# Kernel tuning notes

Hardware: AMD Instinct MI355X
Metric: run time of the kernel (lower is better)

## Reference

```python
import jax, jax.numpy as jnp
import numpy as np

N_NODES = 100000
N_EDGES = 3200000
IN_DIM = 128


def setup_inputs() -> dict:
    key = jax.random.key(0)
    ks = jax.random.split(key, 6)
    x = jax.random.normal(ks[0], (N_NODES, IN_DIM), dtype=jnp.float32)
    edge_index = jax.random.randint(ks[1], (2, N_EDGES), 0, N_NODES, dtype=jnp.int64)
    # Glorot-ish init for weights, zero bias (PyG GCNConv default has bias)
    W1 = jax.random.normal(ks[2], (IN_DIM, 32), dtype=jnp.float32) / np.sqrt(IN_DIM)
    b1 = jnp.zeros((32,), dtype=jnp.float32)
    W2 = jax.random.normal(ks[3], (32, 16), dtype=jnp.float32) / np.sqrt(32.0)
    b2 = jnp.zeros((16,), dtype=jnp.float32)
    Wf = jax.random.normal(ks[4], (16, 1), dtype=jnp.float32) / np.sqrt(16.0)
    bf = jnp.zeros((1,), dtype=jnp.float32)
    return {"x": x, "edge_index": edge_index, "W1": W1, "b1": b1,
            "W2": W2, "b2": b2, "Wf": Wf, "bf": bf}


def reference(x, edge_index, W1, b1, W2, b2, Wf, bf):
    N = x.shape[0]
    # PyG GCNConv: add self-loops, symmetric normalization D^-1/2 (A+I) D^-1/2
    loop = jnp.arange(N, dtype=edge_index.dtype)
    src = jnp.concatenate([edge_index[0], loop])  # message sources (x_j)
    dst = jnp.concatenate([edge_index[1], loop])  # aggregation targets
    deg = jax.ops.segment_sum(jnp.ones_like(dst, dtype=x.dtype), dst, num_segments=N)
    dinv = jax.lax.rsqrt(jnp.maximum(deg, 1.0))  # deg >= 1 due to self-loops
    norm = dinv[src] * dinv[dst]                  # per-edge coefficient

    def gcn_conv(h, W, b):
        h = h @ W                                 # linear transform first (small dim)
        msg = h[src] * norm[:, None]              # gather + scale
        return jax.ops.segment_sum(msg, dst, num_segments=N) + b  # scatter-add

    h = jax.nn.relu(gcn_conv(x, W1, b1))
    h = jax.nn.relu(gcn_conv(h, W2, b2))
    return (h @ Wf + bf).squeeze(-1)              # [N]
```

## Files before the change

### kernel.cpp

```cpp
#include <hip/hip_runtime.h>


#define TPB 256
#define NBUCK 256
#define BCAP 16384
#define CHUNK 8192

__device__ __forceinline__ unsigned f2bf(float f) {
    unsigned u = __float_as_uint(f);
    return (u + 0x7FFFu + ((u >> 16) & 1u)) >> 16;
}
__device__ __forceinline__ float bflo(unsigned u) { return __uint_as_float(u << 16); }
__device__ __forceinline__ float bfhi(unsigned u) { return __uint_as_float(u & 0xFFFF0000u); }

__global__ void zero_bcursor_kernel(int* __restrict__ bcur) {
    bcur[threadIdx.x] = 0;
}

__global__ __launch_bounds__(256) void binA2_kernel(
        const int* __restrict__ src, const int* __restrict__ dst,
        int* __restrict__ bcur, unsigned* __restrict__ staging, int E, int NPB) {
    __shared__ unsigned packed[CHUNK];
    __shared__ unsigned char buckb[CHUNK];
    __shared__ int hist[NBUCK];
    __shared__ int scan_[NBUCK];
    __shared__ int lstart[NBUCK];
    __shared__ int lcur[NBUCK];
    __shared__ int gbase[NBUCK];
    int tid = threadIdx.x;
    int start = blockIdx.x * CHUNK;
    int sz = min(CHUNK, E - start);

    hist[tid] = 0;
    __syncthreads();
    for (int i = tid; i < sz; i += 256) {
        unsigned d = (unsigned)dst[start + i];
        atomicAdd(&hist[d / (unsigned)NPB], 1);
    }
    __syncthreads();
    int v = hist[tid];
    scan_[tid] = v;
    __syncthreads();
    for (int dd = 1; dd < NBUCK; dd <<= 1) {
        int t = 0;
        if (tid >= dd) t = scan_[tid - dd];
        __syncthreads();
        scan_[tid] += t;
        __syncthreads();
    }
    lstart[tid] = scan_[tid] - v;
    lcur[tid] = 0;
    gbase[tid] = atomicAdd(&bcur[tid], v);
    __syncthreads();
    for (int i = tid; i < sz; i += 256) {
        unsigned d = (unsigned)dst[start + i];
        unsigned s = (unsigned)src[start + i];
        unsigned b = d / (unsigned)NPB;
        unsigned loc = d - b * (unsigned)NPB;
        int pos = atomicAdd(&lcur[b], 1);
        int si = lstart[b] + pos;
        packed[si] = (loc << 20) | s;
        buckb[si] = (unsigned char)b;
    }
    __syncthreads();
    for (int i = tid; i < sz; i += 256) {
        unsigned b = buckb[i];
        int dsti = gbase[b] + (i - lstart[b]);
        if (dsti < BCAP)
            staging[(size_t)b * BCAP + dsti] = packed[i];
    }
}

__global__ void bucket_scan_kernel(const int* __restrict__ bcur, int* __restrict__ bbase) {
    __shared__ int s[NBUCK];
    int tid = threadIdx.x;
    int v = min(bcur[tid], BCAP);
    s[tid] = v;
    __syncthreads();
    for (int d = 1; d < NBUCK; d <<= 1) {
        int t = 0;
        if (tid >= d) t = s[tid - d];
        __syncthreads();
        s[tid] += t;
        __syncthreads();
    }
    bbase[tid] = s[tid] - v;
}

__global__ void buildB_kernel(const int* __restrict__ bcur, const int* __restrict__ bbase,
                              const unsigned* __restrict__ staging,
                              int* __restrict__ offs, int* __restrict__ counts,
                              float* __restrict__ dinv, int* __restrict__ csr_src,
                              int N, int NPB) {
    __shared__ int hist[512];
    __shared__ int scan_[512];
    __shared__ int cur[512];
    int b = blockIdx.x;
    int tid = threadIdx.x;
    int sz = min(bcur[b], BCAP);
    int base = bbase[b];
    int n0 = b * NPB;
    int nn = min(NPB, N - n0);
    const unsigned* se = staging + (size_t)b * BCAP;

    hist[tid] = 0;
    __syncthreads();
    for (int i = tid; i < sz; i += 512)
        atomicAdd(&hist[se[i] >> 20], 1);
    __syncthreads();
    int h = hist[tid];
    scan_[tid] = h;
    __syncthreads();
    for (int d = 1; d < 512; d <<= 1) {
        int t = 0;
        if (tid >= d) t = scan_[tid - d];
        __syncthreads();
        scan_[tid] += t;
        __syncthreads();
    }
    int excl = scan_[tid] - h;
    cur[tid] = excl;
    if (tid < nn) {
        int node = n0 + tid;
        offs[node] = base + excl;
        counts[node] = h;
        dinv[node] = rsqrtf((float)(h + 1));
    }
    __syncthreads();
    for (int i = tid; i < sz; i += 512) {
        unsigned p = se[i];
        int pos = atomicAdd(&cur[p >> 20], 1);
        csr_src[base + pos] = (int)(p & 0xFFFFFu);
    }
}

__global__ __launch_bounds__(256) void gemm1_kernel(
        const float* __restrict__ x, const float* __restrict__ W1,
        const float* __restrict__ dinv, unsigned* __restrict__ xwd, int N) {
    __shared__ float ws_[128 * 32];
    for (int i = threadIdx.x; i < 128 * 32; i += blockDim.x) ws_[i] = W1[i];
    __syncthreads();
    int t = threadIdx.x;
    int node = blockIdx.x * 64 + (t >> 2);
    if (node >= N) return;
    int jq = (t & 3) * 8;
    float acc[8];
#pragma unroll
    for (int j = 0; j < 8; ++j) acc[j] = 0.0f;
    const float4* xr = (const float4*)(x + (size_t)node * 128);
#pragma unroll 4
    for (int k4 = 0; k4 < 32; ++k4) {
        float4 xv = xr[k4];
        const float* wb = ws_ + (k4 * 4) * 32 + jq;
        float4 a0 = *(const float4*)(wb);
        float4 a1 = *(const float4*)(wb + 4);
        float4 b0 = *(const float4*)(wb + 32);
        float4 b1v = *(const float4*)(wb + 36);
        float4 c0 = *(const float4*)(wb + 64);
        float4 c1 = *(const float4*)(wb + 68);
        float4 d0 = *(const float4*)(wb + 96);
        float4 d1 = *(const float4*)(wb + 100);
        acc[0] += xv.x * a0.x + xv.y * b0.x + xv.z * c0.x + xv.w * d0.x;
        acc[1] += xv.x * a0.y + xv.y * b0.y + xv.z * c0.y + xv.w * d0.y;
        acc[2] += xv.x * a0.z + xv.y * b0.z + xv.z * c0.z + xv.w * d0.z;
        acc[3] += xv.x * a0.w + xv.y * b0.w + xv.z * c0.w + xv.w * d0.w;
        acc[4] += xv.x * a1.x + xv.y * b1v.x + xv.z * c1.x + xv.w * d1.x;
        acc[5] += xv.x * a1.y + xv.y * b1v.y + xv.z * c1.y + xv.w * d1.y;
        acc[6] += xv.x * a1.z + xv.y * b1v.z + xv.z * c1.z + xv.w * d1.z;
        acc[7] += xv.x * a1.w + xv.y * b1v.w + xv.z * c1.w + xv.w * d1.w;
    }
    float d = dinv[node];
    unsigned pk0 = f2bf(acc[0] * d) | (f2bf(acc[1] * d) << 16);
    unsigned pk1 = f2bf(acc[2] * d) | (f2bf(acc[3] * d) << 16);
    unsigned pk2 = f2bf(acc[4] * d) | (f2bf(acc[5] * d) << 16);
    unsigned pk3 = f2bf(acc[6] * d) | (f2bf(acc[7] * d) << 16);
    ((uint4*)(xwd + (size_t)node * 16))[t & 3] = make_uint4(pk0, pk1, pk2, pk3);
}

__global__ __launch_bounds__(256) void aggS32_kernel(
        const int* __restrict__ offs, const int* __restrict__ counts,
        const int* __restrict__ csr_src, const float* __restrict__ dinv,
        const unsigned* __restrict__ xwd, float* __restrict__ agg, int N) {
    int t = threadIdx.x;
    int q = t & 3;
    int node = blockIdx.x * 64 + (t >> 2);
    if (node >= N) return;
    int off = offs[node];
    int deg = counts[node];
    float acc[8];
    {
        uint4 v = ((const uint4*)(xwd + (size_t)node * 16))[q];
        acc[0] = bflo(v.x); acc[1] = bfhi(v.x);
        acc[2] = bflo(v.y); acc[3] = bfhi(v.y);
        acc[4] = bflo(v.z); acc[5] = bfhi(v.z);
        acc[6] = bflo(v.w); acc[7] = bfhi(v.w);
    }
    int i = 0;
    for (; i + 1 < deg; i += 2) {
        int s0 = csr_src[off + i];
        int s1 = csr_src[off + i + 1];
        uint4 v0 = ((const uint4*)(xwd + (size_t)s0 * 16))[q];
        uint4 v1 = ((const uint4*)(xwd + (size_t)s1 * 16))[q];
        acc[0] += bflo(v0.x) + bflo(v1.x); acc[1] += bfhi(v0.x) + bfhi(v1.x);
        acc[2] += bflo(v0.y) + bflo(v1.y); acc[3] += bfhi(v0.y) + bfhi(v1.y);
        acc[4] += bflo(v0.z) + bflo(v1.z); acc[5] += bfhi(v0.z) + bfhi(v1.z);
        acc[6] += bflo(v0.w) + bflo(v1.w); acc[7] += bfhi(v0.w) + bfhi(v1.w);
    }
    if (i < deg) {
        int s = csr_src[off + i];
        uint4 v = ((const uint4*)(xwd + (size_t)s * 16))[q];
        acc[0] += bflo(v.x); acc[1] += bfhi(v.x);
        acc[2] += bflo(v.y); acc[3] += bfhi(v.y);
        acc[4] += bflo(v.z); acc[5] += bfhi(v.z);
        acc[6] += bflo(v.w); acc[7] += bfhi(v.w);
    }
    float dv = dinv[node];
    float* op = agg + (size_t)node * 32 + q * 8;
    ((float4*)op)[0] = make_float4(acc[0] * dv, acc[1] * dv, acc[2] * dv, acc[3] * dv);
    ((float4*)op)[1] = make_float4(acc[4] * dv, acc[5] * dv, acc[6] * dv, acc[7] * dv);
}

__global__ void gemm2_kernel(const float* __restrict__ agg1, const float* __restrict__ W2,
                             const float* __restrict__ b1, const float* __restrict__ dinv,
                             unsigned* __restrict__ h2wd, int N) {
    __shared__ float ws_[32 * 16];
    __shared__ float bs_[32];
    for (int i = threadIdx.x; i < 32 * 16; i += blockDim.x) ws_[i] = W2[i];
    if (threadIdx.x < 32) bs_[threadIdx.x] = b1[threadIdx.x];
    __syncthreads();
    int node = blockIdx.x * blockDim.x + threadIdx.x;
    if (node >= N) return;
    float h[32];
    const float4* ar = (const float4*)(agg1 + (size_t)node * 32);
#pragma unroll
    for (int k4 = 0; k4 < 8; ++k4) {
        float4 v = ar[k4];
        h[k4 * 4 + 0] = fmaxf(v.x + bs_[k4 * 4 + 0], 0.0f);
        h[k4 * 4 + 1] = fmaxf(v.y + bs_[k4 * 4 + 1], 0.0f);
        h[k4 * 4 + 2] = fmaxf(v.z + bs_[k4 * 4 + 2], 0.0f);
        h[k4 * 4 + 3] = fmaxf(v.w + bs_[k4 * 4 + 3], 0.0f);
    }
    float acc[16];
#pragma unroll
    for (int j = 0; j < 16; ++j) acc[j] = 0.0f;
#pragma unroll
    for (int k = 0; k < 32; ++k) {
        float hv = h[k];
#pragma unroll
        for (int j4 = 0; j4 < 4; ++j4) {
            float4 w = *(const float4*)(ws_ + k * 16 + j4 * 4);
            acc[j4 * 4 + 0] += hv * w.x;
            acc[j4 * 4 + 1] += hv * w.y;
            acc[j4 * 4 + 2] += hv * w.z;
            acc[j4 * 4 + 3] += hv * w.w;
        }
    }
    float d = dinv[node];
    unsigned pk[8];
#pragma unroll
    for (int j = 0; j < 8; ++j)
        pk[j] = f2bf(acc[2 * j] * d) | (f2bf(acc[2 * j + 1] * d) << 16);
    uint4* hp = (uint4*)(h2wd + (size_t)node * 8);
    hp[0] = make_uint4(pk[0], pk[1], pk[2], pk[3]);
    hp[1] = make_uint4(pk[4], pk[5], pk[6], pk[7]);
}

__global__ __launch_bounds__(256) void aggS16f_kernel(
        const int* __restrict__ offs, const int* __restrict__ counts,
        const int* __restrict__ csr_src, const float* __restrict__ dinv,
        const unsigned* __restrict__ h2wd,
        const float* __restrict__ b2, const float* __restrict__ Wf,
        const float* __restrict__ bf, float* __restrict__ out, int N) {
    __shared__ float bs_[16];
    __shared__ float wf_[16];
    __shared__ float bfv;
    int t = threadIdx.x;
    if (t < 16) { bs_[t] = b2[t]; wf_[t] = Wf[t]; }
    if (t == 0) bfv = bf[0];
    __syncthreads();
    int q = t & 1;
    int node = blockIdx.x * 128 + (t >> 1);
    if (node >= N) return;
    int off = offs[node];
    int deg = counts[node];
    float acc[8];
    {
        uint4 v = ((const uint4*)(h2wd + (size_t)node * 8))[q];
        acc[0] = bflo(v.x); acc[1] = bfhi(v.x);
        acc[2] = bflo(v.y); acc[3] = bfhi(v.y);
        acc[4] = bflo(v.z); acc[5] = bfhi(v.z);
        acc[6] = bflo(v.w); acc[7] = bfhi(v.w);
    }
    int i = 0;
    for (; i + 1 < deg; i += 2) {
        int s0 = csr_src[off + i];
        int s1 = csr_src[off + i + 1];
        uint4 v0 = ((const uint4*)(h2wd + (size_t)s0 * 8))[q];
        uint4 v1 = ((const uint4*)(h2wd + (size_t)s1 * 8))[q];
        acc[0] += bflo(v0.x) + bflo(v1.x); acc[1] += bfhi(v0.x) + bfhi(v1.x);
        acc[2] += bflo(v0.y) + bflo(v1.y); acc[3] += bfhi(v0.y) + bfhi(v1.y);
        acc[4] += bflo(v0.z) + bflo(v1.z); acc[5] += bfhi(v0.z) + bfhi(v1.z);
        acc[6] += bflo(v0.w) + bflo(v1.w); acc[7] += bfhi(v0.w) + bfhi(v1.w);
    }
    if (i < deg) {
        int s = csr_src[off + i];
        uint4 v = ((const uint4*)(h2wd + (size_t)s * 8))[q];
        acc[0] += bflo(v.x); acc[1] += bfhi(v.x);
        acc[2] += bflo(v.y); acc[3] += bfhi(v.y);
        acc[4] += bflo(v.z); acc[5] += bfhi(v.z);
        acc[6] += bflo(v.w); acc[7] += bfhi(v.w);
    }
    float dv = dinv[node];
    const float* bq = bs_ + q * 8;
    const float* wq = wf_ + q * 8;
    float part = 0.f;
#pragma unroll
    for (int k = 0; k < 8; ++k)
        part += fmaxf(acc[k] * dv + bq[k], 0.f) * wq[k];
    part += __shfl_xor(part, 1, 64);
    if (q == 0) out[node] = part + bfv;
}

extern "C" void kernel_launch(void* const* d_in, const int* in_sizes, int n_in,
                              void* d_out, int out_size, void* d_ws, size_t ws_size,
                              hipStream_t stream) {
    const float* x  = (const float*)d_in[0];
    const int*   ei = (const int*)d_in[1];
    const float* W1 = (const float*)d_in[2];
    const float* b1 = (const float*)d_in[3];
    const float* W2 = (const float*)d_in[4];
    const float* b2 = (const float*)d_in[5];
    const float* Wf = (const float*)d_in[6];
    const float* bf = (const float*)d_in[7];

    int N = in_sizes[0] / 128;
    int E = in_sizes[1] / 2;
    const int* src = ei;
    const int* dst = ei + E;
    int NPB = (N + NBUCK - 1) / NBUCK;

    size_t Np = ((size_t)N + 3) & ~(size_t)3;
    size_t Ep = ((size_t)E + 3) & ~(size_t)3;
    int* wsI      = (int*)d_ws;
    int* counts   = wsI;
    int* offs     = counts + Np;
    int* bcur     = offs + Np;
    int* bbase    = bcur + NBUCK;
    int* csr_src  = bbase + NBUCK;
    float* dinv   = (float*)(csr_src + Ep);
    unsigned* xwd = (unsigned*)(dinv + Np);
    float* agg1   = (float*)(xwd + 16 * Np);
    unsigned* h2wd= (unsigned*)(agg1 + 32 * Np);
    float* out    = (float*)d_out;
    unsigned* staging = (unsigned*)agg1;

    int nbG1 = (N + 63) / 64;
    int nbC  = (E + CHUNK - 1) / CHUNK;
    int nbN  = (N + TPB - 1) / TPB;
    int nbA32 = (N + 63) / 64;
    int nbA16 = (N + 127) / 128;

    zero_bcursor_kernel<<<1, NBUCK, 0, stream>>>(bcur);
    binA2_kernel<<<nbC, 256, 0, stream>>>(src, dst, bcur, staging, E, NPB);
    bucket_scan_kernel<<<1, NBUCK, 0, stream>>>(bcur, bbase);
    buildB_kernel<<<NBUCK, 512, 0, stream>>>(bcur, bbase, staging, offs, counts,
                                             dinv, csr_src, N, NPB);
    gemm1_kernel<<<nbG1, 256, 0, stream>>>(x, W1, dinv, xwd, N);
    aggS32_kernel<<<nbA32, 256, 0, stream>>>(offs, counts, csr_src, dinv, xwd, agg1, N);
    gemm2_kernel<<<nbN, TPB, 0, stream>>>(agg1, W2, b1, dinv, h2wd, N);
    aggS16f_kernel<<<nbA16, 256, 0, stream>>>(offs, counts, csr_src, dinv, h2wd,
                                              b2, Wf, bf, out, N);
}
```

Before: 284.9 us.

## Split layer-1 features into two half arrays and aggregate each in a separate pass

Gemm1 now writes the 32-wide bf16 projected features as two 16-wide arrays, and layer-1 aggregation runs twice, once per half, with 2 threads per node. Each half array is 3.2 MB rather than 6.4 MB, so the random gathers should hit L2 more often, at the cost of reading the CSR index lists twice. The bucket prefix scan is folded into each buildB block, and the zeroing kernel is replaced by a memset, removing two small launches.

```diff
diff --git a/kernel.cpp b/kernel.cpp
--- a/kernel.cpp
+++ b/kernel.cpp
@@ -12,10 +12,6 @@
 }
 __device__ __forceinline__ float bflo(unsigned u) { return __uint_as_float(u << 16); }
 __device__ __forceinline__ float bfhi(unsigned u) { return __uint_as_float(u & 0xFFFF0000u); }
-
-__global__ void zero_bcursor_kernel(int* __restrict__ bcur) {
-    bcur[threadIdx.x] = 0;
-}
 
 __global__ __launch_bounds__(256) void binA2_kernel(
         const int* __restrict__ src, const int* __restrict__ dst,
@@ -71,34 +67,28 @@
     }
 }
 
-__global__ void bucket_scan_kernel(const int* __restrict__ bcur, int* __restrict__ bbase) {
-    __shared__ int s[NBUCK];
-    int tid = threadIdx.x;
-    int v = min(bcur[tid], BCAP);
-    s[tid] = v;
-    __syncthreads();
-    for (int d = 1; d < NBUCK; d <<= 1) {
-        int t = 0;
-        if (tid >= d) t = s[tid - d];
-        __syncthreads();
-        s[tid] += t;
-        __syncthreads();
-    }
-    bbase[tid] = s[tid] - v;
-}
-
-__global__ void buildB_kernel(const int* __restrict__ bcur, const int* __restrict__ bbase,
+__global__ void buildB_kernel(const int* __restrict__ bcur,
                               const unsigned* __restrict__ staging,
                               int* __restrict__ offs, int* __restrict__ counts,
                               float* __restrict__ dinv, int* __restrict__ csr_src,
                               int N, int NPB) {
+    __shared__ int sb[NBUCK];
     __shared__ int hist[512];
     __shared__ int scan_[512];
     __shared__ int cur[512];
     int b = blockIdx.x;
     int tid = threadIdx.x;
+    if (tid < NBUCK) sb[tid] = min(bcur[tid], BCAP);
+    __syncthreads();
+    for (int d = 1; d < NBUCK; d <<= 1) {
+        int t = 0;
+        if (tid < NBUCK && tid >= d) t = sb[tid - d];
+        __syncthreads();
+        if (tid < NBUCK) sb[tid] += t;
+        __syncthreads();
+    }
     int sz = min(bcur[b], BCAP);
-    int base = bbase[b];
+    int base = (b == 0) ? 0 : sb[b - 1];
     int n0 = b * NPB;
     int nn = min(NPB, N - n0);
     const unsigned* se = staging + (size_t)b * BCAP;
@@ -136,14 +126,16 @@
 
 __global__ __launch_bounds__(256) void gemm1_kernel(
         const float* __restrict__ x, const float* __restrict__ W1,
-        const float* __restrict__ dinv, unsigned* __restrict__ xwd, int N) {
+        const float* __restrict__ dinv, unsigned* __restrict__ xwdA,
+        unsigned* __restrict__ xwdB, int N) {
     __shared__ float ws_[128 * 32];
     for (int i = threadIdx.x; i < 128 * 32; i += blockDim.x) ws_[i] = W1[i];
     __syncthreads();
     int t = threadIdx.x;
     int node = blockIdx.x * 64 + (t >> 2);
     if (node >= N) return;
-    int jq = (t & 3) * 8;
+    int slice = t & 3;
+    int jq = slice * 8;
     float acc[8];
 #pragma unroll
     for (int j = 0; j < 8; ++j) acc[j] = 0.0f;
@@ -174,22 +166,23 @@
     unsigned pk1 = f2bf(acc[2] * d) | (f2bf(acc[3] * d) << 16);
     unsigned pk2 = f2bf(acc[4] * d) | (f2bf(acc[5] * d) << 16);
     unsigned pk3 = f2bf(acc[6] * d) | (f2bf(acc[7] * d) << 16);
-    ((uint4*)(xwd + (size_t)node * 16))[t & 3] = make_uint4(pk0, pk1, pk2, pk3);
-}
-
-__global__ __launch_bounds__(256) void aggS32_kernel(
+    unsigned* dstArr = (slice < 2) ? xwdA : xwdB;
+    ((uint4*)(dstArr + (size_t)node * 8))[slice & 1] = make_uint4(pk0, pk1, pk2, pk3);
+}
+
+__global__ __launch_bounds__(256) void aggH_kernel(
         const int* __restrict__ offs, const int* __restrict__ counts,
         const int* __restrict__ csr_src, const float* __restrict__ dinv,
-        const unsigned* __restrict__ xwd, float* __restrict__ agg, int N) {
+        const unsigned* __restrict__ xh, float* __restrict__ aggHalf, int N) {
     int t = threadIdx.x;
-    int q = t & 3;
-    int node = blockIdx.x * 64 + (t >> 2);
+    int q = t & 1;
+    int node = blockIdx.x * 128 + (t >> 1);
     if (node >= N) return;
     int off = offs[node];
     int deg = counts[node];
     float acc[8];
     {
-        uint4 v = ((const uint4*)(xwd + (size_t)node * 16))[q];
+        uint4 v = ((const uint4*)(xh + (size_t)node * 8))[q];
         acc[0] = bflo(v.x); acc[1] = bfhi(v.x);
         acc[2] = bflo(v.y); acc[3] = bfhi(v.y);
         acc[4] = bflo(v.z); acc[5] = bfhi(v.z);
@@ -199,8 +192,8 @@
     for (; i + 1 < deg; i += 2) {
         int s0 = csr_src[off + i];
         int s1 = csr_src[off + i + 1];
-        uint4 v0 = ((const uint4*)(xwd + (size_t)s0 * 16))[q];
-        uint4 v1 = ((const uint4*)(xwd + (size_t)s1 * 16))[q];
+        uint4 v0 = ((const uint4*)(xh + (size_t)s0 * 8))[q];
+        uint4 v1 = ((const uint4*)(xh + (size_t)s1 * 8))[q];
         acc[0] += bflo(v0.x) + bflo(v1.x); acc[1] += bfhi(v0.x) + bfhi(v1.x);
         acc[2] += bflo(v0.y) + bflo(v1.y); acc[3] += bfhi(v0.y) + bfhi(v1.y);
         acc[4] += bflo(v0.z) + bflo(v1.z); acc[5] += bfhi(v0.z) + bfhi(v1.z);
@@ -208,14 +201,14 @@
     }
     if (i < deg) {
         int s = csr_src[off + i];
-        uint4 v = ((const uint4*)(xwd + (size_t)s * 16))[q];
+        uint4 v = ((const uint4*)(xh + (size_t)s * 8))[q];
         acc[0] += bflo(v.x); acc[1] += bfhi(v.x);
         acc[2] += bflo(v.y); acc[3] += bfhi(v.y);
         acc[4] += bflo(v.z); acc[5] += bfhi(v.z);
         acc[6] += bflo(v.w); acc[7] += bfhi(v.w);
     }
     float dv = dinv[node];
-    float* op = agg + (size_t)node * 32 + q * 8;
+    float* op = aggHalf + (size_t)node * 32 + q * 8;
     ((float4*)op)[0] = make_float4(acc[0] * dv, acc[1] * dv, acc[2] * dv, acc[3] * dv);
     ((float4*)op)[1] = make_float4(acc[4] * dv, acc[5] * dv, acc[6] * dv, acc[7] * dv);
 }
@@ -345,11 +338,11 @@
     int* counts   = wsI;
     int* offs     = counts + Np;
     int* bcur     = offs + Np;
-    int* bbase    = bcur + NBUCK;
-    int* csr_src  = bbase + NBUCK;
+    int* csr_src  = bcur + NBUCK;
     float* dinv   = (float*)(csr_src + Ep);
-    unsigned* xwd = (unsigned*)(dinv + Np);
-    float* agg1   = (float*)(xwd + 16 * Np);
+    unsigned* xwdA= (unsigned*)(dinv + Np);
+    unsigned* xwdB= xwdA + 8 * Np;
+    float* agg1   = (float*)(xwdB + 8 * Np);
     unsigned* h2wd= (unsigned*)(agg1 + 32 * Np);
     float* out    = (float*)d_out;
     unsigned* staging = (unsigned*)agg1;
@@ -357,17 +350,16 @@
     int nbG1 = (N + 63) / 64;
     int nbC  = (E + CHUNK - 1) / CHUNK;
     int nbN  = (N + TPB - 1) / TPB;
-    int nbA32 = (N + 63) / 64;
-    int nbA16 = (N + 127) / 128;
-
-    zero_bcursor_kernel<<<1, NBUCK, 0, stream>>>(bcur);
+    int nbA  = (N + 127) / 128;
+
+    hipMemsetAsync(bcur, 0, NBUCK * sizeof(int), stream);
     binA2_kernel<<<nbC, 256, 0, stream>>>(src, dst, bcur, staging, E, NPB);
-    bucket_scan_kernel<<<1, NBUCK, 0, stream>>>(bcur, bbase);
-    buildB_kernel<<<NBUCK, 512, 0, stream>>>(bcur, bbase, staging, offs, counts,
+    buildB_kernel<<<NBUCK, 512, 0, stream>>>(bcur, staging, offs, counts,
                                              dinv, csr_src, N, NPB);
-    gemm1_kernel<<<nbG1, 256, 0, stream>>>(x, W1, dinv, xwd, N);
-    aggS32_kernel<<<nbA32, 256, 0, stream>>>(offs, counts, csr_src, dinv, xwd, agg1, N);
+    gemm1_kernel<<<nbG1, 256, 0, stream>>>(x, W1, dinv, xwdA, xwdB, N);
+    aggH_kernel<<<nbA, 256, 0, stream>>>(offs, counts, csr_src, dinv, xwdA, agg1, N);
+    aggH_kernel<<<nbA, 256, 0, stream>>>(offs, counts, csr_src, dinv, xwdB, agg1 + 16, N);
     gemm2_kernel<<<nbN, TPB, 0, stream>>>(agg1, W2, b1, dinv, h2wd, N);
-    aggS16f_kernel<<<nbA16, 256, 0, stream>>>(offs, counts, csr_src, dinv, h2wd,
-                                              b2, Wf, bf, out, N);
-}
+    aggS16f_kernel<<<nbA, 256, 0, stream>>>(offs, counts, csr_src, dinv, h2wd,
+                                            b2, Wf, bf, out, N);
+}
```

New measurement: 305.8 us. 7.3% more time.
